# Kernel tuning notes

Measured on AMD Instinct MI355X. Metric: run time of the kernel, lower is better.

## Reference

```python
import jax, jax.numpy as jnp
import numpy as np

B, S, T = 4, 512, 512
V, D, F, H, DK, N = 32000, 512, 2048, 8, 64, 6
PAD = 0

# sinusoidal positional encoding table, matching the torch source exactly
_pos = np.arange(max(S, T))[:, None]
_i = np.arange(D // 2)[None, :]
_ang = _pos / (10000.0 ** (2 * _i / D))
_pe = np.empty((max(S, T), D), dtype=np.float32)
_pe[:, 0::2] = np.sin(_ang)
_pe[:, 1::2] = np.cos(_ang)
PE = jnp.asarray(_pe)


def setup_inputs() -> dict:
    key = jax.random.key(0)
    ks = iter(jax.random.split(key, 64))
    s = 0.02
    w = lambda shape: jax.random.normal(next(ks), shape, jnp.float32) * s
    inp = {
        'src': jax.random.randint(next(ks), (B, S), 0, V, jnp.int32),
        'trg': jax.random.randint(next(ks), (B, T), 0, V, jnp.int32),
        'emb_src': w((V, D)).at[PAD].set(0.0),
        'emb_trg': w((V, D)).at[PAD].set(0.0),
        # encoder stacks (leading axis = layer)
        'enc_wq': w((N, D, H * DK)), 'enc_wk': w((N, D, H * DK)),
        'enc_wv': w((N, D, H * DK)), 'enc_wo': w((N, H * DK, D)),
        'enc_ln1_g': jnp.ones((N, D)), 'enc_ln1_b': jnp.zeros((N, D)),
        'enc_w1': w((N, D, F)), 'enc_b1': jnp.zeros((N, F)),
        'enc_w2': w((N, F, D)), 'enc_b2': jnp.zeros((N, D)),
        'enc_ln2_g': jnp.ones((N, D)), 'enc_ln2_b': jnp.zeros((N, D)),
        # decoder stacks
        'dec_wq': w((N, D, H * DK)), 'dec_wk': w((N, D, H * DK)),
        'dec_wv': w((N, D, H * DK)), 'dec_wo': w((N, H * DK, D)),
        'dec_ln1_g': jnp.ones((N, D)), 'dec_ln1_b': jnp.zeros((N, D)),
        'dec_cq': w((N, D, H * DK)), 'dec_ck': w((N, D, H * DK)),
        'dec_cv': w((N, D, H * DK)), 'dec_co': w((N, H * DK, D)),
        'dec_ln2_g': jnp.ones((N, D)), 'dec_ln2_b': jnp.zeros((N, D)),
        'dec_w1': w((N, D, F)), 'dec_b1': jnp.zeros((N, F)),
        'dec_w2': w((N, F, D)), 'dec_b2': jnp.zeros((N, D)),
        'dec_ln3_g': jnp.ones((N, D)), 'dec_ln3_b': jnp.zeros((N, D)),
        'proj': w((D, V)),
    }
    return inp


def _ln(x, g, b, eps=1e-5):
    m = x.mean(-1, keepdims=True)
    v = ((x - m) ** 2).mean(-1, keepdims=True)
    return (x - m) * jax.lax.rsqrt(v + eps) * g + b


def _mha(xq, xkv, wq, wk, wv, wo, mask):
    b, lq, _ = xq.shape
    lk = xkv.shape[1]
    q = (xq @ wq).reshape(b, lq, H, DK).transpose(0, 2, 1, 3)   # bhqd
    k = (xkv @ wk).reshape(b, lk, H, DK).transpose(0, 2, 1, 3)  # bhkd
    v = (xkv @ wv).reshape(b, lk, H, DK).transpose(0, 2, 1, 3)  # bhkd
    scores = jnp.einsum('bhqd,bhkd->bhqk', q, k)
    scores = jnp.where(mask, -jnp.inf, scores)
    attn = jax.nn.softmax(scores * (DK ** -0.5), axis=-1)
    out = jnp.einsum('bhqk,bhkd->bhqd', attn, v)
    out = out.transpose(0, 2, 1, 3).reshape(b, lq, H * DK)
    return out @ wo


def _ffn(x, w1, b1, w2, b2):
    return jax.nn.relu(x @ w1 + b1) @ w2 + b2


def reference(src, trg, emb_src, emb_trg,
              enc_wq, enc_wk, enc_wv, enc_wo, enc_ln1_g, enc_ln1_b,
              enc_w1, enc_b1, enc_w2, enc_b2, enc_ln2_g, enc_ln2_b,
              dec_wq, dec_wk, dec_wv, dec_wo, dec_ln1_g, dec_ln1_b,
              dec_cq, dec_ck, dec_cv, dec_co, dec_ln2_g, dec_ln2_b,
              dec_w1, dec_b1, dec_w2, dec_b2, dec_ln3_g, dec_ln3_b,
              proj):
    scale = D ** 0.5
    src_pad = (src == PAD)[:, None, None, :]                 # [B,1,1,S]
    trg_pad = (trg == PAD)[:, None, None, :]                 # [B,1,1,T]
    causal = jnp.triu(jnp.ones((T, T), bool), 1)[None, None]  # [1,1,T,T]
    trg_mask = trg_pad | causal

    # encoder (dropout = identity in eval)
    x = emb_src[src] * scale + PE[None, :S]

    def enc_step(h, p):
        wq, wk, wv, wo, g1, b1, w1, bb1, w2, bb2, g2, b2 = p
        h = _ln(h + _mha(h, h, wq, wk, wv, wo, src_pad), g1, b1)
        h = _ln(h + _ffn(h, w1, bb1, w2, bb2), g2, b2)
        return h, None

    x_enc, _ = jax.lax.scan(enc_step, x,
        (enc_wq, enc_wk, enc_wv, enc_wo, enc_ln1_g, enc_ln1_b,
         enc_w1, enc_b1, enc_w2, enc_b2, enc_ln2_g, enc_ln2_b))

    # decoder
    y = emb_trg[trg] * scale + PE[None, :T]

    def dec_step(h, p):
        (wq, wk, wv, wo, g1, b1, cq, ck, cv, co, g2, b2,
         w1, bb1, w2, bb2, g3, b3) = p
        h = _ln(h + _mha(h, h, wq, wk, wv, wo, trg_mask), g1, b1)
        h = _ln(h + _mha(h, x_enc, cq, ck, cv, co, src_pad), g2, b2)
        h = _ln(h + _ffn(h, w1, bb1, w2, bb2), g3, b3)
        return h, None

    y, _ = jax.lax.scan(dec_step, y,
        (dec_wq, dec_wk, dec_wv, dec_wo, dec_ln1_g, dec_ln1_b,
         dec_cq, dec_ck, dec_cv, dec_co, dec_ln2_g, dec_ln2_b,
         dec_w1, dec_b1, dec_w2, dec_b2, dec_ln3_g, dec_ln3_b))

    return y @ proj  # [B, T, trg_vocab]
```

## Files before the change

### kernel.cpp

```cpp
#include <hip/hip_runtime.h>
#include <math.h>

#define BBATCH 4
#define SS 512
#define DDIM 512
#define FFN 2048
#define NHEAD 8
#define DHEAD 64
#define NL 6
#define NVOC 32000
#define MTOK (BBATCH*SS)
#define PAD_ID 0
#define MSZE ((size_t)MTOK * DDIM)

typedef unsigned short u16;
typedef __attribute__((ext_vector_type(8))) short short8;
typedef __attribute__((ext_vector_type(4))) float f32x4;

__device__ __forceinline__ u16 f2bf(float f) {
    union { float f; unsigned u; } v; v.f = f;
    unsigned r = ((v.u >> 16) & 1u) + 0x7fffu;
    return (u16)((v.u + r) >> 16);
}

__device__ __forceinline__ void gload16(const u16* g, u16* l) {
    __builtin_amdgcn_global_load_lds(
        (const __attribute__((address_space(1))) void*)g,
        (__attribute__((address_space(3))) void*)l, 16, 0, 0);
}

template<int N> __device__ __forceinline__ void waitv() {
    if constexpr (N == 0)      asm volatile("s_waitcnt vmcnt(0)" ::: "memory");
    else if constexpr (N == 2) asm volatile("s_waitcnt vmcnt(2)" ::: "memory");
    else if constexpr (N == 3) asm volatile("s_waitcnt vmcnt(3)" ::: "memory");
    else if constexpr (N == 4) asm volatile("s_waitcnt vmcnt(4)" ::: "memory");
    else if constexpr (N == 6) asm volatile("s_waitcnt vmcnt(6)" ::: "memory");
    else if constexpr (N == 8) asm volatile("s_waitcnt vmcnt(8)" ::: "memory");
    __builtin_amdgcn_sched_barrier(0);
}
__device__ __forceinline__ void rawbar() {
    __builtin_amdgcn_s_barrier();
    __builtin_amdgcn_sched_barrier(0);
}

template<int BM, int BN, int OUTBF, int RELU, int BIAS>
__device__ __forceinline__ void gemm_core(
    u16* __restrict__ AsB, u16* __restrict__ BsB,
    const u16* __restrict__ A, int lda,
    const u16* __restrict__ B, int ldb,
    void* __restrict__ Cv, int ldc,
    int row0, int col0, int K, const float* __restrict__ bias)
{
    const int tid  = threadIdx.x;
    const int lane = tid & 63;
    const int wid  = tid >> 6;
    const int wr   = wid >> 1, wc = wid & 1;
    constexpr int MF = BM / 32, NF = BN / 32, RA = BM / 64, RB = BN / 64;
// ... 102 lines not shown
        int nwg = gridDim.x * gridDim.y;
        int lin = by * gridDim.x + bx;
        int cpx = nwg >> 3;
        int s = (lin & 7) * cpx + (lin >> 3);
        bx = s % gridDim.x; by = s / gridDim.x;
    }
    const int zb = blockIdx.z >> 3, zh = blockIdx.z & 7;
    const u16* Ab = A + (size_t)zb * aSb + (size_t)zh * aSh;
    const u16* Bb = B + (size_t)zb * bSb + (size_t)zh * bSh;
    void* Cb = OUTBF ? (void*)((u16*)Cv + (size_t)zb * cSb + (size_t)zh * cSh)
                     : (void*)((float*)Cv + (size_t)zb * cSb + (size_t)zh * cSh);
    gemm_core<BM, BN, OUTBF, RELU, BIAS>(As, Bs, Ab, lda, Bb, ldb, Cb, ldc,
                                          by * BM, bx * BN, K, bias);
}

template<int BM, int BN>
__global__ __launch_bounds__(256) void mgemm_dual(
    const u16* __restrict__ A1, int lda1, const u16* __restrict__ B1, int ldb1,
    u16* __restrict__ C1, int ldc1, int nx1, int nblk1,
    const u16* __restrict__ A2, int lda2, const u16* __restrict__ B2, int ldb2,
    u16* __restrict__ C2, int ldc2, int nx2,
    int K)
{
    __shared__ __align__(16) u16 As[4 * BM * 32];
    __shared__ __align__(16) u16 Bs[4 * BN * 32];
    int id = blockIdx.x;
    if (id < nblk1) {
        gemm_core<BM, BN, 1, 0, 0>(As, Bs, A1, lda1, B1, ldb1, C1, ldc1,
                                    (id / nx1) * BM, (id % nx1) * BN, K, nullptr);
    } else {
        id -= nblk1;
        gemm_core<BM, BN, 1, 0, 0>(As, Bs, A2, lda2, B2, ldb2, C2, ldc2,
                                    (id / nx2) * BM, (id % nx2) * BN, K, nullptr);
    }
}

template<int CAUSAL>
__global__ __launch_bounds__(512) void flash_attn(
    const u16* __restrict__ Qp, int ldq,
    const u16* __restrict__ Kp, int ldk,
    const u16* __restrict__ Vtp,
    u16* __restrict__ O,
    const int* __restrict__ ids)
{
    __shared__ __align__(16) u16 Kl[3][64 * 64];
    __shared__ __align__(16) u16 Vl[3][64 * 64];
    __shared__ __align__(16) u16 Pl[8][16 * 64];
    __shared__ float msk[SS];

    const int tid = threadIdx.x, lane = tid & 63, wid = tid >> 6;
    const int bh = blockIdx.y, b = bh >> 3, h = bh & 7;
    const int q0 = blockIdx.x * 128;

    for (int i = tid; i < SS; i += 512)
        msk[i] = (ids[b * SS + i] == PAD_ID) ? -1e30f : 0.0f;

    const int qloc = wid * 16 + (lane & 15);
    const u16* Qb = Qp + (size_t)(b * SS + q0 + qloc) * ldq + h * 64 + ((lane >> 4) * 8);
    short8 qf[2];
    qf[0] = *(const short8*)(Qb);
    qf[1] = *(const short8*)(Qb + 32);

    const u16* Kb = Kp + (size_t)b * SS * ldk + h * 64;
    const u16* Vb = Vtp + (size_t)(h * 64) * MTOK + b * SS;

    auto stage = [&](int buf, int kt) {
        int row = tid >> 3;
        int sl  = tid & 7;
        int ls = sl ^ (row & 7);
        gload16(Kb + (size_t)(kt * 64 + row) * ldk + ls * 8, &Kl[buf][row * 64 + sl * 8]);
        gload16(Vb + (size_t)row * MTOK + kt * 64 + ls * 8, &Vl[buf][row * 64 + sl * 8]);
    };

    const int nt = CAUSAL ? (2 * blockIdx.x + 2) : (SS / 64);

    float m_i[4], l_i[4];
    f32x4 o_acc[4];
    const f32x4 zero = {0.f, 0.f, 0.f, 0.f};
    #pragma unroll
    for (int i = 0; i < 4; i++) { m_i[i] = -1e30f; l_i[i] = 0.0f; }
    #pragma unroll
    for (int n = 0; n < 4; n++) o_acc[n] = zero;

    auto comp = [&](int kt) {
        const int cur = kt % 3;
        f32x4 s_acc[4];
        #pragma unroll
        for (int n = 0; n < 4; n++) s_acc[n] = zero;
        __builtin_amdgcn_s_setprio(1);
        #pragma unroll
        for (int kk = 0; kk < 2; kk++) {
            #pragma unroll
            for (int n = 0; n < 4; n++) {
                int row = n * 16 + (lane & 15);
                int ls = (kk * 4 + (lane >> 4)) ^ (row & 7);
                short8 kf = *(const short8*)&Kl[cur][row * 64 + ls * 8];
                s_acc[n] = __builtin_amdgcn_mfma_f32_16x16x32_bf16(qf[kk], kf, s_acc[n], 0, 0, 0);
            }
        }
        __builtin_amdgcn_s_setprio(0);

        float sv[4][4];
        #pragma unroll
        for (int n = 0; n < 4; n++) {
            int kg = kt * 64 + n * 16 + (lane & 15);
            float mk = msk[kg];
            #pragma unroll
            for (int i = 0; i < 4; i++) {
                float s = s_acc[n][i] * 0.125f + mk;
                if (CAUSAL) {
                    int qg = q0 + wid * 16 + ((lane >> 4) << 2) + i;
// ... 29 lines not shown
                ps[i] += __shfl_xor(ps[i], msh);
            l_i[i] = l_i[i] * rs[i] + ps[i];
        }
        #pragma unroll
        for (int n = 0; n < 4; n++)
            #pragma unroll
            for (int i = 0; i < 4; i++)
                o_acc[n][i] *= rs[i];

        #pragma unroll
        for (int n = 0; n < 4; n++) {
            int k = n * 16 + (lane & 15);
            #pragma unroll
            for (int i = 0; i < 4; i++) {
                int q = ((lane >> 4) << 2) + i;
                Pl[wid][q * 64 + (((k >> 3) ^ (q & 7)) << 3) + (k & 7)] = f2bf(p[n][i]);
            }
        }
        asm volatile("s_waitcnt lgkmcnt(0)" ::: "memory");
        __builtin_amdgcn_sched_barrier(0);

        __builtin_amdgcn_s_setprio(1);
        #pragma unroll
        for (int kk = 0; kk < 2; kk++) {
            int qrow = lane & 15;
            int lsp = (kk * 4 + (lane >> 4)) ^ (qrow & 7);
            short8 pa = *(const short8*)&Pl[wid][qrow * 64 + lsp * 8];
            #pragma unroll
            for (int nf = 0; nf < 4; nf++) {
                int row = nf * 16 + (lane & 15);
                int vs = (kk * 4 + (lane >> 4)) ^ (row & 7);
                short8 vf = *(const short8*)&Vl[cur][row * 64 + vs * 8];
                o_acc[nf] = __builtin_amdgcn_mfma_f32_16x16x32_bf16(pa, vf, o_acc[nf], 0, 0, 0);
            }
        }
        __builtin_amdgcn_s_setprio(0);
    };

    stage(0, 0);
    stage(1, 1);
    int t = 0;
    for (; t < nt - 1; ++t) {
        waitv<2>();
        rawbar();
        if (t + 2 < nt) stage((t + 2) % 3, t + 2);
        comp(t);
    }
    waitv<0>(); rawbar(); comp(nt - 1);

    #pragma unroll
    for (int nf = 0; nf < 4; nf++) {
        int d = h * 64 + nf * 16 + (lane & 15);
        #pragma unroll
        for (int i = 0; i < 4; i++) {
            int qg = b * SS + q0 + wid * 16 + ((lane >> 4) << 2) + i;
            O[(size_t)qg * DDIM + d] = f2bf(o_acc[nf][i] / l_i[i]);
        }
    }
}

__device__ __forceinline__ void transp_core(const float* __restrict__ src, u16* __restrict__ dst,
                                            int N, int K, int n0, int k0)
{
    __shared__ u16 t[64][65];
    const int tid = threadIdx.x;
    #pragma unroll
    for (int i = 0; i < 16; i++) {
        int idx = tid + i * 256;
        int kr = idx >> 6, nc = idx & 63;
        t[kr][nc] = f2bf(src[(size_t)(k0 + kr) * N + n0 + nc]);
    }
    __syncthreads();
    #pragma unroll
    for (int i = 0; i < 16; i++) {
        int idx = tid + i * 256;
        int nr = idx >> 6, kc = idx & 63;
        dst[(size_t)(n0 + nr) * K + k0 + kc] = t[kc][nr];
    }
}

__global__ __launch_bounds__(256) void transp(const float* __restrict__ src, u16* __restrict__ dst,
                                              int N, int K, size_t sStride, size_t dStride)
{
    transp_core(src + (size_t)blockIdx.z * sStride, dst + (size_t)blockIdx.z * dStride,
                N, K, blockIdx.x * 64, blockIdx.y * 64);
}

#define OFF_QK 0u
#define OFF_WV 524288u
#define OFF_WO 786432u
#define OFF_CQ 1048576u
#define OFF_CK 1310720u
#define OFF_CV 1572864u
#define OFF_CO 1835008u
#define OFF_W1 2097152u
#define OFF_W2 3145728u
#define WBLK   4194304u
#define M2CNT  262144u
#define MF1CNT 1048576u

__global__ __launch_bounds__(256) void transpW(
    const float* p0, const float* p1, const float* p2, const float* p3,
    const float* p4, const float* p5, const float* p6, const float* p7,
    const float* p8, const float* p9, const float* p10, const float* p11,
    u16* __restrict__ wreg)
{
    int z = blockIdx.z;
    int w = z % 12, l = z / 12;
    const float* ptrs[12] = {p0,p1,p2,p3,p4,p5,p6,p7,p8,p9,p10,p11};
    const float* src = ptrs[w] + (size_t)l * M2CNT;
    u16* dst = wreg + (w < 4 ? (size_t)l * WBLK + (size_t)w * M2CNT
                             : (size_t)(NL + l) * WBLK + (size_t)(w - 4) * M2CNT);
    transp_core(src, dst, 512, 512, blockIdx.x * 64, blockIdx.y * 64);
}

// ... 3 lines not shown
    int z = blockIdx.z; int l = z % NL, w = z / NL;
    const float* src = (w ? d : e) + (size_t)l * MF1CNT;
    u16* dst = wreg + (size_t)(w * NL + l) * WBLK + OFF_W1;
    transp_core(src, dst, 2048, 512, blockIdx.x * 64, blockIdx.y * 64);
}

__global__ __launch_bounds__(256) void transpF2(const float* __restrict__ e,
                                                const float* __restrict__ d, u16* __restrict__ wreg)
{
    int z = blockIdx.z; int l = z % NL, w = z / NL;
    const float* src = (w ? d : e) + (size_t)l * MF1CNT;
    u16* dst = wreg + (size_t)(w * NL + l) * WBLK + OFF_W2;
    transp_core(src, dst, 512, 2048, blockIdx.x * 64, blockIdx.y * 64);
}

__global__ void pe_kernel(float* __restrict__ PEt)
{
    int pos = blockIdx.x, d = threadIdx.x;
    int i = d >> 1;
    double freq = exp(-(2.0 * (double)i / (double)DDIM) * log(10000.0));
    double ang = (double)pos * freq;
    PEt[pos * DDIM + d] = (float)((d & 1) ? cos(ang) : sin(ang));
}

__global__ void embed_kernel(const int* __restrict__ src, const int* __restrict__ trg,
                             const float* __restrict__ es, const float* __restrict__ et,
                             const float* __restrict__ PEt,
                             float* __restrict__ X, u16* __restrict__ Xb,
                             float* __restrict__ Y, u16* __restrict__ Ybf)
{
    int gtok = blockIdx.x;
    int d = threadIdx.x;
    bool dec = gtok >= MTOK;
    int tok = dec ? gtok - MTOK : gtok;
    int pos = tok & (SS - 1);
    int id = (dec ? trg : src)[tok];
    const float* emb = dec ? et : es;
    float val = emb[(size_t)id * DDIM + d] * 22.62741699796952f + PEt[pos * DDIM + d];
    (dec ? Y : X)[(size_t)tok * DDIM + d] = val;
    (dec ? Ybf : Xb)[(size_t)tok * DDIM + d] = f2bf(val);
}

__global__ __launch_bounds__(256) void add_ln_kernel(float* __restrict__ x,
    const float* __restrict__ addv, const float* __restrict__ g,
    const float* __restrict__ bta, u16* __restrict__ xb)
{
    int row = blockIdx.x;
    int tid = threadIdx.x;
    size_t base = (size_t)row * DDIM;
    __shared__ float sbuf[4];

    float v0 = x[base + tid]       + addv[base + tid];
    float v1 = x[base + tid + 256] + addv[base + tid + 256];

    float s = v0 + v1;
    #pragma unroll
    for (int o = 32; o > 0; o >>= 1) s += __shfl_down(s, o);
    if ((tid & 63) == 0) sbuf[tid >> 6] = s;
    __syncthreads();
    float mean = (sbuf[0] + sbuf[1] + sbuf[2] + sbuf[3]) * (1.0f / DDIM);
    __syncthreads();

    float d0 = v0 - mean, d1 = v1 - mean;
    float ss = d0 * d0 + d1 * d1;
    #pragma unroll
    for (int o = 32; o > 0; o >>= 1) ss += __shfl_down(ss, o);
    if ((tid & 63) == 0) sbuf[tid >> 6] = ss;
    __syncthreads();
    float var = (sbuf[0] + sbuf[1] + sbuf[2] + sbuf[3]) * (1.0f / DDIM);
    float inv = rsqrtf(var + 1e-5f);

    float o0 = d0 * inv * g[tid]       + bta[tid];
    float o1 = d1 * inv * g[tid + 256] + bta[tid + 256];
    x[base + tid] = o0;
    x[base + tid + 256] = o1;
    xb[base + tid] = f2bf(o0);
    xb[base + tid + 256] = f2bf(o1);
}

__global__ __launch_bounds__(256) void add_ln_red(float* __restrict__ x,
    const float* __restrict__ part, const float* __restrict__ bias,
    const float* __restrict__ g, const float* __restrict__ bta, u16* __restrict__ xb)
{
    int row = blockIdx.x;
    int tid = threadIdx.x;
    size_t base = (size_t)row * DDIM;
    __shared__ float sbuf[4];

    float v0 = x[base + tid]       + bias[tid];
    float v1 = x[base + tid + 256] + bias[tid + 256];
    #pragma unroll
    for (int s4 = 0; s4 < 4; s4++) {
        v0 += part[s4 * MSZE + base + tid];
        v1 += part[s4 * MSZE + base + tid + 256];
    }

    float s = v0 + v1;
    #pragma unroll
    for (int o = 32; o > 0; o >>= 1) s += __shfl_down(s, o);
    if ((tid & 63) == 0) sbuf[tid >> 6] = s;
    __syncthreads();
    float mean = (sbuf[0] + sbuf[1] + sbuf[2] + sbuf[3]) * (1.0f / DDIM);
    __syncthreads();

    float d0 = v0 - mean, d1 = v1 - mean;
    float ss = d0 * d0 + d1 * d1;
    #pragma unroll
    for (int o = 32; o > 0; o >>= 1) ss += __shfl_down(ss, o);
    if ((tid & 63) == 0) sbuf[tid >> 6] = ss;
    __syncthreads();
    float var = (sbuf[0] + sbuf[1] + sbuf[2] + sbuf[3]) * (1.0f / DDIM);
    float inv = rsqrtf(var + 1e-5f);

    float o0 = d0 * inv * g[tid]       + bta[tid];
    float o1 = d1 * inv * g[tid + 256] + bta[tid + 256];
    x[base + tid] = o0;
    x[base + tid + 256] = o1;
    xb[base + tid] = f2bf(o0);
    xb[base + tid + 256] = f2bf(o1);
}

extern "C" void kernel_launch(void* const* d_in, const int* in_sizes, int n_in,
                              void* d_out, int out_size, void* d_ws, size_t ws_size,
                              hipStream_t stream)
{
    (void)in_sizes; (void)n_in; (void)out_size;

    const int*   src      = (const int*)  d_in[0];
    const int*   trg      = (const int*)  d_in[1];
    const float* emb_src  = (const float*)d_in[2];
    const float* emb_trg  = (const float*)d_in[3];
    const float* enc_wq   = (const float*)d_in[4];
    const float* enc_wk   = (const float*)d_in[5];
    const float* enc_wv   = (const float*)d_in[6];
// ... 20 lines not shown
    const float* dec_ln2b = (const float*)d_in[27];
    const float* dec_w1   = (const float*)d_in[28];
    const float* dec_b1   = (const float*)d_in[29];
    const float* dec_w2   = (const float*)d_in[30];
    const float* dec_b2   = (const float*)d_in[31];
    const float* dec_ln3g = (const float*)d_in[32];
    const float* dec_ln3b = (const float*)d_in[33];
    const float* proj     = (const float*)d_in[34];

    float* OUT = (float*)d_out;
    char* base = (char*)d_ws;

    size_t off = 0;
    auto carve = [&](size_t bytes) { char* p = base + off; off += (bytes + 255) & ~(size_t)255; return p; };

    float* X      = (float*)carve(MSZE * 4);
    float* Yb     = (float*)carve(MSZE * 4);
    float* T1     = (float*)carve(MSZE * 4);
    u16*   Xb     = (u16*)  carve(MSZE * 2);
    u16*   Ybf    = (u16*)  carve(MSZE * 2);
    u16*   QKb    = (u16*)  carve((size_t)MTOK * 1024 * 2);
    u16*   Vt     = (u16*)  carve((size_t)512 * MTOK * 2);
    u16*   CTX    = (u16*)  carve(MSZE * 2);
    u16*   HFF    = (u16*)  carve((size_t)MTOK * FFN * 2);
    u16*   Kcr    = (u16*)  carve((size_t)NL * MTOK * 512 * 2);
    u16*   Vtc    = (u16*)  carve((size_t)NL * 512 * MTOK * 2);
    u16*   projT  = (u16*)  carve((size_t)NVOC * 512 * 2);
    float* PEt    = (float*)carve((size_t)SS * DDIM * 4);
    float* Tp4    = (float*)carve((size_t)4 * MSZE * 4);

    const size_t WFULL_B = (size_t)12 * WBLK * 2;
    bool full = (ws_size >= off + WFULL_B);
    u16* Wreg = (u16*)carve(full ? WFULL_B : (size_t)WBLK * 2);

    auto T = [&](const float* s, u16* d, int Kd, int Nd, size_t ss, size_t ds, int L) {
        transp<<<dim3(Nd / 64, Kd / 64, L), 256, 0, stream>>>(s, d, Nd, Kd, ss, ds);
    };

    pe_kernel<<<SS, DDIM, 0, stream>>>(PEt);
    T(proj, projT, 512, NVOC, 0, 0, 1);
    if (full) {
        transpW<<<dim3(8, 8, 12 * NL), 256, 0, stream>>>(
            enc_wq, enc_wk, enc_wv, enc_wo,
            dec_wq, dec_wk, dec_wv, dec_wo,
            dec_cq, dec_ck, dec_cv, dec_co, Wreg);
        transpF1<<<dim3(32, 8, 2 * NL), 256, 0, stream>>>(enc_w1, dec_w1, Wreg);
        transpF2<<<dim3(8, 32, 2 * NL), 256, 0, stream>>>(enc_w2, dec_w2, Wreg);
    }
    embed_kernel<<<2 * MTOK, DDIM, 0, stream>>>(src, trg, emb_src, emb_trg, PEt, X, Xb, Yb, Ybf);

    auto self_attn = [&](const u16* xsrc, const u16* wb, const int* mask_ids, int causal) {
        mgemm_dual<128, 128><<<dim3(192), 256, 0, stream>>>(
            xsrc, 512, wb + OFF_QK, 512, QKb, 1024, 8, 128,
            wb + OFF_WV, 512, xsrc, 512, Vt, MTOK, 16,
            512);
        if (causal)
            flash_attn<1><<<dim3(4, 32), 512, 0, stream>>>(QKb, 1024, QKb + 512, 1024, Vt, CTX, mask_ids);
        else
            flash_attn<0><<<dim3(4, 32), 512, 0, stream>>>(QKb, 1024, QKb + 512, 1024, Vt, CTX, mask_ids);
        mgemm<64, 64, 0, 0, 0><<<dim3(8, 32, 1), 256, 0, stream>>>(
            CTX, 512, 0, 0, wb + OFF_WO, 512, 0, 0, T1, 512, 0, 0, 512, nullptr);
    };

    auto ffn = [&](const u16* xsrc, const u16* wb, const float* b1) {
        mgemm<128, 128, 1, 1, 1><<<dim3(16, 16, 1), 256, 0, stream>>>(
            xsrc, 512, 0, 0, wb + OFF_W1, 512, 0, 0, HFF, FFN, 0, 0, 512, b1);
        mgemm<128, 128, 0, 0, 0><<<dim3(4, 16, 4), 256, 0, stream>>>(
            HFF, 2048, 0, 512, wb + OFF_W2, 2048, 0, 512,
            Tp4, 512, 0, MSZE, 512, nullptr);
    };

    const size_t M2 = M2CNT, MF1 = MF1CNT;

    for (int l = 0; l < NL; l++) {
        u16* wb;
        if (full) wb = Wreg + (size_t)l * WBLK;
        else {
            wb = Wreg;
            T(enc_wq + l * M2,  wb + OFF_QK,          512, 512,  0, 0, 1);
            T(enc_wk + l * M2,  wb + OFF_QK + M2,     512, 512,  0, 0, 1);
            T(enc_wv + l * M2,  wb + OFF_WV,          512, 512,  0, 0, 1);
            T(enc_wo + l * M2,  wb + OFF_WO,          512, 512,  0, 0, 1);
            T(enc_w1 + l * MF1, wb + OFF_W1,          512, 2048, 0, 0, 1);
            T(enc_w2 + l * MF1, wb + OFF_W2,          2048, 512, 0, 0, 1);
        }
        self_attn(Xb, wb, src, 0);
        add_ln_kernel<<<MTOK, 256, 0, stream>>>(X, T1, enc_ln1g + l * DDIM, enc_ln1b + l * DDIM, Xb);
        ffn(Xb, wb, enc_b1 + l * FFN);
        add_ln_red<<<MTOK, 256, 0, stream>>>(X, Tp4, enc_b2 + l * DDIM,
                                             enc_ln2g + l * DDIM, enc_ln2b + l * DDIM, Xb);
    }

    if (full) {
        u16* Wd = Wreg + (size_t)NL * WBLK;
        mgemm<128, 128, 1, 0, 0><<<dim3(4, 16, NL), 256, 0, stream>>>(
            Xb, 512, 0, 0, Wd + OFF_CK, 512, 0, WBLK, Kcr, 512, 0, (size_t)MTOK * 512, 512, nullptr);
        mgemm<128, 128, 1, 0, 0><<<dim3(16, 4, NL), 256, 0, stream>>>(
            Wd + OFF_CV, 512, 0, WBLK, Xb, 512, 0, 0, Vtc, MTOK, 0, (size_t)512 * MTOK, 512, nullptr);
    }

    for (int l = 0; l < NL; l++) {
        u16* wb;
        if (full) wb = Wreg + (size_t)(NL + l) * WBLK;
        else {
            wb = Wreg;
            T(dec_wq + l * M2,  wb + OFF_QK,          512, 512,  0, 0, 1);
            T(dec_wk + l * M2,  wb + OFF_QK + M2,     512, 512,  0, 0, 1);
            T(dec_wv + l * M2,  wb + OFF_WV,          512, 512,  0, 0, 1);
            T(dec_wo + l * M2,  wb + OFF_WO,          512, 512,  0, 0, 1);
            T(dec_cq + l * M2,  wb + OFF_CQ,          512, 512,  0, 0, 1);
            T(dec_ck + l * M2,  wb + OFF_CK,          512, 512,  0, 0, 1);
            T(dec_cv + l * M2,  wb + OFF_CV,          512, 512,  0, 0, 1);
            T(dec_co + l * M2,  wb + OFF_CO,          512, 512,  0, 0, 1);
            T(dec_w1 + l * MF1, wb + OFF_W1,          512, 2048, 0, 0, 1);
            T(dec_w2 + l * MF1, wb + OFF_W2,          2048, 512, 0, 0, 1);
            mgemm<128, 128, 1, 0, 0><<<dim3(4, 16, 1), 256, 0, stream>>>(
                Xb, 512, 0, 0, wb + OFF_CK, 512, 0, 0, Kcr + (size_t)l * MTOK * 512, 512, 0, 0, 512, nullptr);
            mgemm<128, 128, 1, 0, 0><<<dim3(16, 4, 1), 256, 0, stream>>>(
                wb + OFF_CV, 512, 0, 0, Xb, 512, 0, 0, Vtc + (size_t)l * 512 * MTOK, MTOK, 0, 0, 512, nullptr);
        }
        self_attn(Ybf, wb, trg, 1);
        add_ln_kernel<<<MTOK, 256, 0, stream>>>(Yb, T1, dec_ln1g + l * DDIM, dec_ln1b + l * DDIM, Ybf);
        mgemm<64, 64, 1, 0, 0><<<dim3(8, 32, 1), 256, 0, stream>>>(
            Ybf, 512, 0, 0, wb + OFF_CQ, 512, 0, 0, QKb, 1024, 0, 0, 512, nullptr);
        flash_attn<0><<<dim3(4, 32), 512, 0, stream>>>(
            QKb, 1024, Kcr + (size_t)l * MTOK * 512, 512, Vtc + (size_t)l * 512 * MTOK, CTX, src);
        mgemm<64, 64, 0, 0, 0><<<dim3(8, 32, 1), 256, 0, stream>>>(
            CTX, 512, 0, 0, wb + OFF_CO, 512, 0, 0, T1, 512, 0, 0, 512, nullptr);
        add_ln_kernel<<<MTOK, 256, 0, stream>>>(Yb, T1, dec_ln2g + l * DDIM, dec_ln2b + l * DDIM, Ybf);
        ffn(Ybf, wb, dec_b1 + l * FFN);
        add_ln_red<<<MTOK, 256, 0, stream>>>(Yb, Tp4, dec_b2 + l * DDIM,
                                             dec_ln3g + l * DDIM, dec_ln3b + l * DDIM, Ybf);
    }

    mgemm<128, 128, 0, 0, 0, 1><<<dim3(NVOC / 128, 16, 1), 256, 0, stream>>>(
        Ybf, 512, 0, 0, projT, 512, 0, 0, OUT, NVOC, 0, 0, 512, nullptr);
}
```

Before: 1.547 ms.

## Fuse each encoder/decoder layer into one persistent kernel with grid barriers

Replaces the per-layer chain of separate GEMM, flash-attention and layernorm launches with a single 256-block persistent kernel per layer. Phases are separated by atomic-counter grid barriers in global memory. Flash attention is reworked to 256 threads and 64-row query tiles so it fits the same block shape, and the positional-encoding kernel is removed from the launch sequence. This is meant to cut launch overhead and inter-kernel gaps, at the cost of spin-wait barriers that need all 256 blocks co-resident and of less flexible per-phase tiling.

```diff
diff --git a/kernel.cpp b/kernel.cpp
--- a/kernel.cpp
+++ b/kernel.cpp
@@ -32,15 +32,25 @@
 template<int N> __device__ __forceinline__ void waitv() {
     if constexpr (N == 0)      asm volatile("s_waitcnt vmcnt(0)" ::: "memory");
     else if constexpr (N == 2) asm volatile("s_waitcnt vmcnt(2)" ::: "memory");
-    else if constexpr (N == 3) asm volatile("s_waitcnt vmcnt(3)" ::: "memory");
     else if constexpr (N == 4) asm volatile("s_waitcnt vmcnt(4)" ::: "memory");
-    else if constexpr (N == 6) asm volatile("s_waitcnt vmcnt(6)" ::: "memory");
     else if constexpr (N == 8) asm volatile("s_waitcnt vmcnt(8)" ::: "memory");
     __builtin_amdgcn_sched_barrier(0);
 }
 __device__ __forceinline__ void rawbar() {
     __builtin_amdgcn_s_barrier();
     __builtin_amdgcn_sched_barrier(0);
+}
+
+__device__ __forceinline__ void gbar(unsigned* c) {
+    __threadfence();
+    __syncthreads();
+    if (threadIdx.x == 0) {
+        __hip_atomic_fetch_add(c, 1u, __ATOMIC_ACQ_REL, __HIP_MEMORY_SCOPE_AGENT);
+        while (__hip_atomic_load(c, __ATOMIC_ACQUIRE, __HIP_MEMORY_SCOPE_AGENT) < 256u)
+            __builtin_amdgcn_s_sleep(2);
+        __threadfence();
+    }
+    __syncthreads();
 }
 
 template<int BM, int BN, int OUTBF, int RELU, int BIAS>
@@ -173,45 +183,23 @@
                                           by * BM, bx * BN, K, bias);
 }
 
-template<int BM, int BN>
-__global__ __launch_bounds__(256) void mgemm_dual(
-    const u16* __restrict__ A1, int lda1, const u16* __restrict__ B1, int ldb1,
-    u16* __restrict__ C1, int ldc1, int nx1, int nblk1,
-    const u16* __restrict__ A2, int lda2, const u16* __restrict__ B2, int ldb2,
-    u16* __restrict__ C2, int ldc2, int nx2,
-    int K)
-{
-    __shared__ __align__(16) u16 As[4 * BM * 32];
-    __shared__ __align__(16) u16 Bs[4 * BN * 32];
-    int id = blockIdx.x;
-    if (id < nblk1) {
-        gemm_core<BM, BN, 1, 0, 0>(As, Bs, A1, lda1, B1, ldb1, C1, ldc1,
-                                    (id / nx1) * BM, (id % nx1) * BN, K, nullptr);
-    } else {
-        id -= nblk1;
-        gemm_core<BM, BN, 1, 0, 0>(As, Bs, A2, lda2, B2, ldb2, C2, ldc2,
-                                    (id / nx2) * BM, (id % nx2) * BN, K, nullptr);
-    }
-}
-
 template<int CAUSAL>
-__global__ __launch_bounds__(512) void flash_attn(
+__device__ void flash_phase(char* smem, int qt, int bh,
     const u16* __restrict__ Qp, int ldq,
     const u16* __restrict__ Kp, int ldk,
     const u16* __restrict__ Vtp,
-    u16* __restrict__ O,
-    const int* __restrict__ ids)
-{
-    __shared__ __align__(16) u16 Kl[3][64 * 64];
-    __shared__ __align__(16) u16 Vl[3][64 * 64];
-    __shared__ __align__(16) u16 Pl[8][16 * 64];
-    __shared__ float msk[SS];
+    u16* __restrict__ O, const int* __restrict__ ids)
+{
+    u16* Kl = (u16*)smem;
+    u16* Vl = Kl + 12288;
+    u16* Pl = Vl + 12288;
+    float* msk = (float*)(Pl + 4096);
 
     const int tid = threadIdx.x, lane = tid & 63, wid = tid >> 6;
-    const int bh = blockIdx.y, b = bh >> 3, h = bh & 7;
-    const int q0 = blockIdx.x * 128;
-
-    for (int i = tid; i < SS; i += 512)
+    const int b = bh >> 3, h = bh & 7;
+    const int q0 = qt * 64;
+
+    for (int i = tid; i < SS; i += 256)
         msk[i] = (ids[b * SS + i] == PAD_ID) ? -1e30f : 0.0f;
 
     const int qloc = wid * 16 + (lane & 15);
@@ -220,18 +208,22 @@
     qf[0] = *(const short8*)(Qb);
     qf[1] = *(const short8*)(Qb + 32);
 
-    const u16* Kb = Kp + (size_t)b * SS * ldk + h * 64;
+    const u16* Kb = Qp == Kp ? Kp : Kp;
+    Kb = Kp + (size_t)b * SS * ldk + h * 64;
     const u16* Vb = Vtp + (size_t)(h * 64) * MTOK + b * SS;
 
     auto stage = [&](int buf, int kt) {
-        int row = tid >> 3;
-        int sl  = tid & 7;
-        int ls = sl ^ (row & 7);
-        gload16(Kb + (size_t)(kt * 64 + row) * ldk + ls * 8, &Kl[buf][row * 64 + sl * 8]);
-        gload16(Vb + (size_t)row * MTOK + kt * 64 + ls * 8, &Vl[buf][row * 64 + sl * 8]);
+        int row = tid >> 3, sl = tid & 7;
+        #pragma unroll
+        for (int r = 0; r < 2; r++) {
+            int rr = row + r * 32;
+            int ls = sl ^ (rr & 7);
+            gload16(Kb + (size_t)(kt * 64 + rr) * ldk + ls * 8, &Kl[buf * 4096 + rr * 64 + sl * 8]);
+            gload16(Vb + (size_t)rr * MTOK + kt * 64 + ls * 8, &Vl[buf * 4096 + rr * 64 + sl * 8]);
+        }
     };
 
-    const int nt = CAUSAL ? (2 * blockIdx.x + 2) : (SS / 64);
+    const int nt = CAUSAL ? (qt + 1) : (SS / 64);
 
     float m_i[4], l_i[4];
     f32x4 o_acc[4];
@@ -253,7 +245,7 @@
             for (int n = 0; n < 4; n++) {
                 int row = n * 16 + (lane & 15);
                 int ls = (kk * 4 + (lane >> 4)) ^ (row & 7);
-                short8 kf = *(const short8*)&Kl[cur][row * 64 + ls * 8];
+                short8 kf = *(const short8*)&Kl[cur * 4096 + row * 64 + ls * 8];
                 s_acc[n] = __builtin_amdgcn_mfma_f32_16x16x32_bf16(qf[kk], kf, s_acc[n], 0, 0, 0);
             }
         }
@@ -313,7 +305,7 @@
             #pragma unroll
             for (int i = 0; i < 4; i++) {
                 int q = ((lane >> 4) << 2) + i;
-                Pl[wid][q * 64 + (((k >> 3) ^ (q & 7)) << 3) + (k & 7)] = f2bf(p[n][i]);
+                Pl[wid * 1024 + q * 64 + (((k >> 3) ^ (q & 7)) << 3) + (k & 7)] = f2bf(p[n][i]);
             }
         }
         asm volatile("s_waitcnt lgkmcnt(0)" ::: "memory");
@@ -324,12 +316,12 @@
         for (int kk = 0; kk < 2; kk++) {
             int qrow = lane & 15;
             int lsp = (kk * 4 + (lane >> 4)) ^ (qrow & 7);
-            short8 pa = *(const short8*)&Pl[wid][qrow * 64 + lsp * 8];
+            short8 pa = *(const short8*)&Pl[wid * 1024 + qrow * 64 + lsp * 8];
             #pragma unroll
             for (int nf = 0; nf < 4; nf++) {
                 int row = nf * 16 + (lane & 15);
                 int vs = (kk * 4 + (lane >> 4)) ^ (row & 7);
-                short8 vf = *(const short8*)&Vl[cur][row * 64 + vs * 8];
+                short8 vf = *(const short8*)&Vl[cur * 4096 + row * 64 + vs * 8];
                 o_acc[nf] = __builtin_amdgcn_mfma_f32_16x16x32_bf16(pa, vf, o_acc[nf], 0, 0, 0);
             }
         }
@@ -340,7 +332,7 @@
     stage(1, 1);
     int t = 0;
     for (; t < nt - 1; ++t) {
-        waitv<2>();
+        waitv<4>();
         rawbar();
         if (t + 2 < nt) stage((t + 2) % 3, t + 2);
         comp(t);
@@ -358,31 +350,77 @@
     }
 }
 
-__device__ __forceinline__ void transp_core(const float* __restrict__ src, u16* __restrict__ dst,
-                                            int N, int K, int n0, int k0)
-{
-    __shared__ u16 t[64][65];
+__device__ void ln8(float* __restrict__ x, const float* __restrict__ addv,
+    const float* __restrict__ g, const float* __restrict__ bta,
+    u16* __restrict__ xb, int jid, float* sbuf)
+{
     const int tid = threadIdx.x;
-    #pragma unroll
-    for (int i = 0; i < 16; i++) {
-        int idx = tid + i * 256;
-        int kr = idx >> 6, nc = idx & 63;
-        t[kr][nc] = f2bf(src[(size_t)(k0 + kr) * N + n0 + nc]);
-    }
-    __syncthreads();
-    #pragma unroll
-    for (int i = 0; i < 16; i++) {
-        int idx = tid + i * 256;
-        int nr = idx >> 6, kc = idx & 63;
-        dst[(size_t)(n0 + nr) * K + k0 + kc] = t[kc][nr];
-    }
-}
-
-__global__ __launch_bounds__(256) void transp(const float* __restrict__ src, u16* __restrict__ dst,
-                                              int N, int K, size_t sStride, size_t dStride)
-{
-    transp_core(src + (size_t)blockIdx.z * sStride, dst + (size_t)blockIdx.z * dStride,
-                N, K, blockIdx.x * 64, blockIdx.y * 64);
+    for (int r = 0; r < 8; r++) {
+        size_t base = (size_t)(jid * 8 + r) * DDIM;
+        float v0 = x[base + tid]       + addv[base + tid];
+        float v1 = x[base + tid + 256] + addv[base + tid + 256];
+        float s = v0 + v1;
+        #pragma unroll
+        for (int o = 32; o > 0; o >>= 1) s += __shfl_down(s, o);
+        if ((tid & 63) == 0) sbuf[tid >> 6] = s;
+        __syncthreads();
+        float mean = (sbuf[0] + sbuf[1] + sbuf[2] + sbuf[3]) * (1.0f / DDIM);
+        __syncthreads();
+        float d0 = v0 - mean, d1 = v1 - mean;
+        float ss = d0 * d0 + d1 * d1;
+        #pragma unroll
+        for (int o = 32; o > 0; o >>= 1) ss += __shfl_down(ss, o);
+        if ((tid & 63) == 0) sbuf[tid >> 6] = ss;
+        __syncthreads();
+        float var = (sbuf[0] + sbuf[1] + sbuf[2] + sbuf[3]) * (1.0f / DDIM);
+        float inv = rsqrtf(var + 1e-5f);
+        float o0 = d0 * inv * g[tid]       + bta[tid];
+        float o1 = d1 * inv * g[tid + 256] + bta[tid + 256];
+        x[base + tid] = o0;
+        x[base + tid + 256] = o1;
+        xb[base + tid] = f2bf(o0);
+        xb[base + tid + 256] = f2bf(o1);
+        __syncthreads();
+    }
+}
+
+__device__ void ln_red8(float* __restrict__ x, const float* __restrict__ part,
+    const float* __restrict__ bias, const float* __restrict__ g,
+    const float* __restrict__ bta, u16* __restrict__ xb, int jid, float* sbuf)
+{
+    const int tid = threadIdx.x;
+    for (int r = 0; r < 8; r++) {
+        size_t base = (size_t)(jid * 8 + r) * DDIM;
+        float v0 = x[base + tid]       + bias[tid];
+        float v1 = x[base + tid + 256] + bias[tid + 256];
+        #pragma unroll
+        for (int s4 = 0; s4 < 4; s4++) {
+            v0 += part[s4 * MSZE + base + tid];
+            v1 += part[s4 * MSZE + base + tid + 256];
+        }
+        float s = v0 + v1;
+        #pragma unroll
+        for (int o = 32; o > 0; o >>= 1) s += __shfl_down(s, o);
+        if ((tid & 63) == 0) sbuf[tid >> 6] = s;
+        __syncthreads();
+        float mean = (sbuf[0] + sbuf[1] + sbuf[2] + sbuf[3]) * (1.0f / DDIM);
+        __syncthreads();
+        float d0 = v0 - mean, d1 = v1 - mean;
+        float ss = d0 * d0 + d1 * d1;
+        #pragma unroll
+        for (int o = 32; o > 0; o >>= 1) ss += __shfl_down(ss, o);
+        if ((tid & 63) == 0) sbuf[tid >> 6] = ss;
+        __syncthreads();
+        float var = (sbuf[0] + sbuf[1] + sbuf[2] + sbuf[3]) * (1.0f / DDIM);
+        float inv = rsqrtf(var + 1e-5f);
+        float o0 = d0 * inv * g[tid]       + bta[tid];
+        float o1 = d1 * inv * g[tid + 256] + bta[tid + 256];
+        x[base + tid] = o0;
+        x[base + tid + 256] = o1;
+        xb[base + tid] = f2bf(o0);
+        xb[base + tid + 256] = f2bf(o1);
+        __syncthreads();
+    }
 }
 
 #define OFF_QK 0u
@@ -398,6 +436,125 @@
 #define M2CNT  262144u
 #define MF1CNT 1048576u
 
+__global__ __launch_bounds__(256) void enc_layer(
+    u16* __restrict__ Xb_, float* __restrict__ X_,
+    const u16* __restrict__ wb,
+    const float* __restrict__ b1, const float* __restrict__ b2,
+    const float* __restrict__ ln1g, const float* __restrict__ ln1b,
+    const float* __restrict__ ln2g, const float* __restrict__ ln2b,
+    u16* __restrict__ QKb, u16* __restrict__ Vt, u16* __restrict__ CTX,
+    float* __restrict__ T1, u16* __restrict__ HFF, float* __restrict__ Tp4,
+    const int* __restrict__ ids, unsigned* __restrict__ bar)
+{
+    __shared__ __align__(16) char smem[65536];
+    __shared__ float sbuf[4];
+    u16* A_ = (u16*)smem;  u16* B_ = A_ + 16384;
+    u16* A64 = (u16*)smem; u16* B64 = A64 + 8192;
+    const int jid = blockIdx.x;
+
+    if (jid < 128)
+        gemm_core<128,128,1,0,0>(A_, B_, Xb_, 512, wb + OFF_QK, 512, QKb, 1024,
+                                 (jid >> 3) * 128, (jid & 7) * 128, 512, nullptr);
+    else if (jid < 192)
+        gemm_core<128,128,1,0,0>(A_, B_, wb + OFF_WV, 512, Xb_, 512, Vt, MTOK,
+                                 ((jid - 128) >> 4) * 128, ((jid - 128) & 15) * 128, 512, nullptr);
+    gbar(bar + 0);
+    flash_phase<0>(smem, jid & 7, jid >> 3, QKb, 1024, QKb + 512, 1024, Vt, CTX, ids);
+    gbar(bar + 1);
+    gemm_core<64,64,0,0,0>(A64, B64, CTX, 512, wb + OFF_WO, 512, T1, 512,
+                           (jid >> 3) * 64, (jid & 7) * 64, 512, nullptr);
+    gbar(bar + 2);
+    ln8(X_, T1, ln1g, ln1b, Xb_, jid, sbuf);
+    gbar(bar + 3);
+    gemm_core<128,128,1,1,1>(A_, B_, Xb_, 512, wb + OFF_W1, 512, HFF, FFN,
+                             (jid >> 4) * 128, (jid & 15) * 128, 512, b1);
+    gbar(bar + 4);
+    { int s = jid >> 6, rem = jid & 63;
+      gemm_core<128,128,0,0,0>(A_, B_, HFF + s * 512, 2048, wb + OFF_W2 + s * 512, 2048,
+                               Tp4 + (size_t)s * MSZE, 512, (rem >> 2) * 128, (rem & 3) * 128, 512, nullptr); }
+    gbar(bar + 5);
+    ln_red8(X_, Tp4, b2, ln2g, ln2b, Xb_, jid, sbuf);
+}
+
+__global__ __launch_bounds__(256) void dec_layer(
+    u16* __restrict__ Ybf_, float* __restrict__ Y_,
+    const u16* __restrict__ wb,
+    const float* __restrict__ b1, const float* __restrict__ b2,
+    const float* __restrict__ ln1g, const float* __restrict__ ln1b,
+    const float* __restrict__ ln2g, const float* __restrict__ ln2b,
+    const float* __restrict__ ln3g, const float* __restrict__ ln3b,
+    const u16* __restrict__ Kcr_l, const u16* __restrict__ Vtc_l,
+    u16* __restrict__ QKb, u16* __restrict__ Vt, u16* __restrict__ CTX,
+    float* __restrict__ T1, u16* __restrict__ HFF, float* __restrict__ Tp4,
+    const int* __restrict__ trg, const int* __restrict__ srcids, unsigned* __restrict__ bar)
+{
+    __shared__ __align__(16) char smem[65536];
+    __shared__ float sbuf[4];
+    u16* A_ = (u16*)smem;  u16* B_ = A_ + 16384;
+    u16* A64 = (u16*)smem; u16* B64 = A64 + 8192;
+    const int jid = blockIdx.x;
+
+    if (jid < 128)
+        gemm_core<128,128,1,0,0>(A_, B_, Ybf_, 512, wb + OFF_QK, 512, QKb, 1024,
+                                 (jid >> 3) * 128, (jid & 7) * 128, 512, nullptr);
+    else if (jid < 192)
+        gemm_core<128,128,1,0,0>(A_, B_, wb + OFF_WV, 512, Ybf_, 512, Vt, MTOK,
+                                 ((jid - 128) >> 4) * 128, ((jid - 128) & 15) * 128, 512, nullptr);
+    gbar(bar + 0);
+    flash_phase<1>(smem, jid & 7, jid >> 3, QKb, 1024, QKb + 512, 1024, Vt, CTX, trg);
+    gbar(bar + 1);
+    gemm_core<64,64,0,0,0>(A64, B64, CTX, 512, wb + OFF_WO, 512, T1, 512,
+                           (jid >> 3) * 64, (jid & 7) * 64, 512, nullptr);
+    gbar(bar + 2);
+    ln8(Y_, T1, ln1g, ln1b, Ybf_, jid, sbuf);
+    gbar(bar + 3);
+    gemm_core<64,64,1,0,0>(A64, B64, Ybf_, 512, wb + OFF_CQ, 512, QKb, 1024,
+                           (jid >> 3) * 64, (jid & 7) * 64, 512, nullptr);
+    gbar(bar + 4);
+    flash_phase<0>(smem, jid & 7, jid >> 3, QKb, 1024, Kcr_l, 512, Vtc_l, CTX, srcids);
+    gbar(bar + 5);
+    gemm_core<64,64,0,0,0>(A64, B64, CTX, 512, wb + OFF_CO, 512, T1, 512,
+                           (jid >> 3) * 64, (jid & 7) * 64, 512, nullptr);
+    gbar(bar + 6);
+    ln8(Y_, T1, ln2g, ln2b, Ybf_, jid, sbuf);
+    gbar(bar + 7);
+    gemm_core<128,128,1,1,1>(A_, B_, Ybf_, 512, wb + OFF_W1, 512, HFF, FFN,
+                             (jid >> 4) * 128, (jid & 15) * 128, 512, b1);
+    gbar(bar + 8);
+    { int s = jid >> 6, rem = jid & 63;
+      gemm_core<128,128,0,0,0>(A_, B_, HFF + s * 512, 2048, wb + OFF_W2 + s * 512, 2048,
+                               Tp4 + (size_t)s * MSZE, 512, (rem >> 2) * 128, (rem & 3) * 128, 512, nullptr); }
+    gbar(bar + 9);
+    ln_red8(Y_, Tp4, b2, ln3g, ln3b, Ybf_, jid, sbuf);
+}
+
+__device__ __forceinline__ void transp_core(const float* __restrict__ src, u16* __restrict__ dst,
+                                            int N, int K, int n0, int k0)
+{
+    __shared__ u16 t[64][65];
+    const int tid = threadIdx.x;
+    #pragma unroll
+    for (int i = 0; i < 16; i++) {
+        int idx = tid + i * 256;
+        int kr = idx >> 6, nc = idx & 63;
+        t[kr][nc] = f2bf(src[(size_t)(k0 + kr) * N + n0 + nc]);
+    }
+    __syncthreads();
+    #pragma unroll
+    for (int i = 0; i < 16; i++) {
+        int idx = tid + i * 256;
+        int nr = idx >> 6, kc = idx & 63;
+        dst[(size_t)(n0 + nr) * K + k0 + kc] = t[kc][nr];
+    }
+}
+
+__global__ __launch_bounds__(256) void transp(const float* __restrict__ src, u16* __restrict__ dst,
+                                              int N, int K, size_t sStride, size_t dStride)
+{
+    transp_core(src + (size_t)blockIdx.z * sStride, dst + (size_t)blockIdx.z * dStride,
+                N, K, blockIdx.x * 64, blockIdx.y * 64);
+}
+
 __global__ __launch_bounds__(256) void transpW(
     const float* p0, const float* p1, const float* p2, const float* p3,
     const float* p4, const float* p5, const float* p6, const float* p7,
@@ -431,18 +588,8 @@
     transp_core(src, dst, 512, 2048, blockIdx.x * 64, blockIdx.y * 64);
 }
 
-__global__ void pe_kernel(float* __restrict__ PEt)
-{
-    int pos = blockIdx.x, d = threadIdx.x;
-    int i = d >> 1;
-    double freq = exp(-(2.0 * (double)i / (double)DDIM) * log(10000.0));
-    double ang = (double)pos * freq;
-    PEt[pos * DDIM + d] = (float)((d & 1) ? cos(ang) : sin(ang));
-}
-
 __global__ void embed_kernel(const int* __restrict__ src, const int* __restrict__ trg,
                              const float* __restrict__ es, const float* __restrict__ et,
-                             const float* __restrict__ PEt,
                              float* __restrict__ X, u16* __restrict__ Xb,
                              float* __restrict__ Y, u16* __restrict__ Ybf)
 {
@@ -453,88 +600,13 @@
     int pos = tok & (SS - 1);
     int id = (dec ? trg : src)[tok];
     const float* emb = dec ? et : es;
-    float val = emb[(size_t)id * DDIM + d] * 22.62741699796952f + PEt[pos * DDIM + d];
+    int i = d >> 1;
+    double freq = exp(-(2.0 * (double)i / (double)DDIM) * log(10000.0));
+    double ang = (double)pos * freq;
+    float pe = (float)((d & 1) ? cos(ang) : sin(ang));
+    float val = emb[(size_t)id * DDIM + d] * 22.62741699796952f + pe;
     (dec ? Y : X)[(size_t)tok * DDIM + d] = val;
     (dec ? Ybf : Xb)[(size_t)tok * DDIM + d] = f2bf(val);
-}
-
-__global__ __launch_bounds__(256) void add_ln_kernel(float* __restrict__ x,
-    const float* __restrict__ addv, const float* __restrict__ g,
-    const float* __restrict__ bta, u16* __restrict__ xb)
-{
-    int row = blockIdx.x;
-    int tid = threadIdx.x;
-    size_t base = (size_t)row * DDIM;
-    __shared__ float sbuf[4];
-
-    float v0 = x[base + tid]       + addv[base + tid];
-    float v1 = x[base + tid + 256] + addv[base + tid + 256];
-
-    float s = v0 + v1;
-    #pragma unroll
-    for (int o = 32; o > 0; o >>= 1) s += __shfl_down(s, o);
-    if ((tid & 63) == 0) sbuf[tid >> 6] = s;
-    __syncthreads();
-    float mean = (sbuf[0] + sbuf[1] + sbuf[2] + sbuf[3]) * (1.0f / DDIM);
-    __syncthreads();
-
-    float d0 = v0 - mean, d1 = v1 - mean;
-    float ss = d0 * d0 + d1 * d1;
-    #pragma unroll
-    for (int o = 32; o > 0; o >>= 1) ss += __shfl_down(ss, o);
-    if ((tid & 63) == 0) sbuf[tid >> 6] = ss;
-    __syncthreads();
-    float var = (sbuf[0] + sbuf[1] + sbuf[2] + sbuf[3]) * (1.0f / DDIM);
-    float inv = rsqrtf(var + 1e-5f);
-
-    float o0 = d0 * inv * g[tid]       + bta[tid];
-    float o1 = d1 * inv * g[tid + 256] + bta[tid + 256];
-    x[base + tid] = o0;
-    x[base + tid + 256] = o1;
-    xb[base + tid] = f2bf(o0);
-    xb[base + tid + 256] = f2bf(o1);
-}
-
-__global__ __launch_bounds__(256) void add_ln_red(float* __restrict__ x,
-    const float* __restrict__ part, const float* __restrict__ bias,
-    const float* __restrict__ g, const float* __restrict__ bta, u16* __restrict__ xb)
-{
-    int row = blockIdx.x;
-    int tid = threadIdx.x;
-    size_t base = (size_t)row * DDIM;
-    __shared__ float sbuf[4];
-
-    float v0 = x[base + tid]       + bias[tid];
-    float v1 = x[base + tid + 256] + bias[tid + 256];
-    #pragma unroll
-    for (int s4 = 0; s4 < 4; s4++) {
-        v0 += part[s4 * MSZE + base + tid];
-        v1 += part[s4 * MSZE + base + tid + 256];
-    }
-
-    float s = v0 + v1;
-    #pragma unroll
-    for (int o = 32; o > 0; o >>= 1) s += __shfl_down(s, o);
-    if ((tid & 63) == 0) sbuf[tid >> 6] = s;
-    __syncthreads();
-    float mean = (sbuf[0] + sbuf[1] + sbuf[2] + sbuf[3]) * (1.0f / DDIM);
-    __syncthreads();
-
-    float d0 = v0 - mean, d1 = v1 - mean;
-    float ss = d0 * d0 + d1 * d1;
-    #pragma unroll
-    for (int o = 32; o > 0; o >>= 1) ss += __shfl_down(ss, o);
-    if ((tid & 63) == 0) sbuf[tid >> 6] = ss;
-    __syncthreads();
-    float var = (sbuf[0] + sbuf[1] + sbuf[2] + sbuf[3]) * (1.0f / DDIM);
-    float inv = rsqrtf(var + 1e-5f);
-
-    float o0 = d0 * inv * g[tid]       + bta[tid];
-    float o1 = d1 * inv * g[tid + 256] + bta[tid + 256];
-    x[base + tid] = o0;
-    x[base + tid + 256] = o1;
-    xb[base + tid] = f2bf(o0);
-    xb[base + tid + 256] = f2bf(o1);
 }
 
 extern "C" void kernel_launch(void* const* d_in, const int* in_sizes, int n_in,
@@ -585,20 +657,20 @@
     size_t off = 0;
     auto carve = [&](size_t bytes) { char* p = base + off; off += (bytes + 255) & ~(size_t)255; return p; };
 
-    float* X      = (float*)carve(MSZE * 4);
-    float* Yb     = (float*)carve(MSZE * 4);
-    float* T1     = (float*)carve(MSZE * 4);
-    u16*   Xb     = (u16*)  carve(MSZE * 2);
-    u16*   Ybf    = (u16*)  carve(MSZE * 2);
-    u16*   QKb    = (u16*)  carve((size_t)MTOK * 1024 * 2);
-    u16*   Vt     = (u16*)  carve((size_t)512 * MTOK * 2);
-    u16*   CTX    = (u16*)  carve(MSZE * 2);
-    u16*   HFF    = (u16*)  carve((size_t)MTOK * FFN * 2);
-    u16*   Kcr    = (u16*)  carve((size_t)NL * MTOK * 512 * 2);
-    u16*   Vtc    = (u16*)  carve((size_t)NL * 512 * MTOK * 2);
-    u16*   projT  = (u16*)  carve((size_t)NVOC * 512 * 2);
-    float* PEt    = (float*)carve((size_t)SS * DDIM * 4);
-    float* Tp4    = (float*)carve((size_t)4 * MSZE * 4);
+    float*    X      = (float*)   carve(MSZE * 4);
+    float*    Yb     = (float*)   carve(MSZE * 4);
+    float*    T1     = (float*)   carve(MSZE * 4);
+    u16*      Xb     = (u16*)     carve(MSZE * 2);
+    u16*      Ybf    = (u16*)     carve(MSZE * 2);
+    u16*      QKb    = (u16*)     carve((size_t)MTOK * 1024 * 2);
+    u16*      Vt     = (u16*)     carve((size_t)512 * MTOK * 2);
+    u16*      CTX    = (u16*)     carve(MSZE * 2);
+    u16*      HFF    = (u16*)     carve((size_t)MTOK * FFN * 2);
+    u16*      Kcr    = (u16*)     carve((size_t)NL * MTOK * 512 * 2);
+    u16*      Vtc    = (u16*)     carve((size_t)NL * 512 * MTOK * 2);
+    u16*      projT  = (u16*)     carve((size_t)NVOC * 512 * 2);
+    float*    Tp4    = (float*)   carve((size_t)4 * MSZE * 4);
+    unsigned* Bar    = (unsigned*)carve(12 * 16 * sizeof(unsigned));
 
     const size_t WFULL_B = (size_t)12 * WBLK * 2;
     bool full = (ws_size >= off + WFULL_B);
@@ -608,7 +680,7 @@
         transp<<<dim3(Nd / 64, Kd / 64, L), 256, 0, stream>>>(s, d, Nd, Kd, ss, ds);
     };
 
-    pe_kernel<<<SS, DDIM, 0, stream>>>(PEt);
+    hipMemsetAsync(Bar, 0, 12 * 16 * sizeof(unsigned), stream);
     T(proj, projT, 512, NVOC, 0, 0, 1);
     if (full) {
         transpW<<<dim3(8, 8, 12 * NL), 256, 0, stream>>>(
@@ -618,28 +690,7 @@
         transpF1<<<dim3(32, 8, 2 * NL), 256, 0, stream>>>(enc_w1, dec_w1, Wreg);
         transpF2<<<dim3(8, 32, 2 * NL), 256, 0, stream>>>(enc_w2, dec_w2, Wreg);
     }
-    embed_kernel<<<2 * MTOK, DDIM, 0, stream>>>(src, trg, emb_src, emb_trg, PEt, X, Xb, Yb, Ybf);
-
-    auto self_attn = [&](const u16* xsrc, const u16* wb, const int* mask_ids, int causal) {
-        mgemm_dual<128, 128><<<dim3(192), 256, 0, stream>>>(
-            xsrc, 512, wb + OFF_QK, 512, QKb, 1024, 8, 128,
-            wb + OFF_WV, 512, xsrc, 512, Vt, MTOK, 16,
-            512);
-        if (causal)
-            flash_attn<1><<<dim3(4, 32), 512, 0, stream>>>(QKb, 1024, QKb + 512, 1024, Vt, CTX, mask_ids);
-        else
-            flash_attn<0><<<dim3(4, 32), 512, 0, stream>>>(QKb, 1024, QKb + 512, 1024, Vt, CTX, mask_ids);
-        mgemm<64, 64, 0, 0, 0><<<dim3(8, 32, 1), 256, 0, stream>>>(
-            CTX, 512, 0, 0, wb + OFF_WO, 512, 0, 0, T1, 512, 0, 0, 512, nullptr);
-    };
-
-    auto ffn = [&](const u16* xsrc, const u16* wb, const float* b1) {
-        mgemm<128, 128, 1, 1, 1><<<dim3(16, 16, 1), 256, 0, stream>>>(
-            xsrc, 512, 0, 0, wb + OFF_W1, 512, 0, 0, HFF, FFN, 0, 0, 512, b1);
-        mgemm<128, 128, 0, 0, 0><<<dim3(4, 16, 4), 256, 0, stream>>>(
-            HFF, 2048, 0, 512, wb + OFF_W2, 2048, 0, 512,
-            Tp4, 512, 0, MSZE, 512, nullptr);
-    };
+    embed_kernel<<<2 * MTOK, DDIM, 0, stream>>>(src, trg, emb_src, emb_trg, X, Xb, Yb, Ybf);
 
     const size_t M2 = M2CNT, MF1 = MF1CNT;
 
@@ -648,18 +699,16 @@
         if (full) wb = Wreg + (size_t)l * WBLK;
         else {
             wb = Wreg;
-            T(enc_wq + l * M2,  wb + OFF_QK,          512, 512,  0, 0, 1);
-            T(enc_wk + l * M2,  wb + OFF_QK + M2,     512, 512,  0, 0, 1);
-            T(enc_wv + l * M2,  wb + OFF_WV,          512, 512,  0, 0, 1);
-            T(enc_wo + l * M2,  wb + OFF_WO,          512, 512,  0, 0, 1);
-            T(enc_w1 + l * MF1, wb + OFF_W1,          512, 2048, 0, 0, 1);
-            T(enc_w2 + l * MF1, wb + OFF_W2,          2048, 512, 0, 0, 1);
-        }
-        self_attn(Xb, wb, src, 0);
-        add_ln_kernel<<<MTOK, 256, 0, stream>>>(X, T1, enc_ln1g + l * DDIM, enc_ln1b + l * DDIM, Xb);
-        ffn(Xb, wb, enc_b1 + l * FFN);
-        add_ln_red<<<MTOK, 256, 0, stream>>>(X, Tp4, enc_b2 + l * DDIM,
-                                             enc_ln2g + l * DDIM, enc_ln2b + l * DDIM, Xb);
+            T(enc_wq + l * M2,  wb + OFF_QK,      512, 512,  0, 0, 1);
+            T(enc_wk + l * M2,  wb + OFF_QK + M2, 512, 512,  0, 0, 1);
+            T(enc_wv + l * M2,  wb + OFF_WV,      512, 512,  0, 0, 1);
+            T(enc_wo + l * M2,  wb + OFF_WO,      512, 512,  0, 0, 1);
+            T(enc_w1 + l * MF1, wb + OFF_W1,      512, 2048, 0, 0, 1);
+            T(enc_w2 + l * MF1, wb + OFF_W2,      2048, 512, 0, 0, 1);
+        }
+        enc_layer<<<256, 256, 0, stream>>>(Xb, X, wb, enc_b1 + l * FFN, enc_b2 + l * DDIM,
+            enc_ln1g + l * DDIM, enc_ln1b + l * DDIM, enc_ln2g + l * DDIM, enc_ln2b + l * DDIM,
+            QKb, Vt, CTX, T1, HFF, Tp4, src, Bar + l * 16);
     }
 
     if (full) {
@@ -675,33 +724,26 @@
         if (full) wb = Wreg + (size_t)(NL + l) * WBLK;
         else {
             wb = Wreg;
-            T(dec_wq + l * M2,  wb + OFF_QK,          512, 512,  0, 0, 1);
-            T(dec_wk + l * M2,  wb + OFF_QK + M2,     512, 512,  0, 0, 1);
-            T(dec_wv + l * M2,  wb + OFF_WV,          512, 512,  0, 0, 1);
-            T(dec_wo + l * M2,  wb + OFF_WO,          512, 512,  0, 0, 1);
-            T(dec_cq + l * M2,  wb + OFF_CQ,          512, 512,  0, 0, 1);
-            T(dec_ck + l * M2,  wb + OFF_CK,          512, 512,  0, 0, 1);
-            T(dec_cv + l * M2,  wb + OFF_CV,          512, 512,  0, 0, 1);
-            T(dec_co + l * M2,  wb + OFF_CO,          512, 512,  0, 0, 1);
-            T(dec_w1 + l * MF1, wb + OFF_W1,          512, 2048, 0, 0, 1);
-            T(dec_w2 + l * MF1, wb + OFF_W2,          2048, 512, 0, 0, 1);
+            T(dec_wq + l * M2,  wb + OFF_QK,      512, 512,  0, 0, 1);
+            T(dec_wk + l * M2,  wb + OFF_QK + M2, 512, 512,  0, 0, 1);
+            T(dec_wv + l * M2,  wb + OFF_WV,      512, 512,  0, 0, 1);
+            T(dec_wo + l * M2,  wb + OFF_WO,      512, 512,  0, 0, 1);
+            T(dec_cq + l * M2,  wb + OFF_CQ,      512, 512,  0, 0, 1);
+            T(dec_ck + l * M2,  wb + OFF_CK,      512, 512,  0, 0, 1);
+            T(dec_cv + l * M2,  wb + OFF_CV,      512, 512,  0, 0, 1);
+            T(dec_co + l * M2,  wb + OFF_CO,      512, 512,  0, 0, 1);
+            T(dec_w1 + l * MF1, wb + OFF_W1,      512, 2048, 0, 0, 1);
+            T(dec_w2 + l * MF1, wb + OFF_W2,      2048, 512, 0, 0, 1);
             mgemm<128, 128, 1, 0, 0><<<dim3(4, 16, 1), 256, 0, stream>>>(
                 Xb, 512, 0, 0, wb + OFF_CK, 512, 0, 0, Kcr + (size_t)l * MTOK * 512, 512, 0, 0, 512, nullptr);
             mgemm<128, 128, 1, 0, 0><<<dim3(16, 4, 1), 256, 0, stream>>>(
                 wb + OFF_CV, 512, 0, 0, Xb, 512, 0, 0, Vtc + (size_t)l * 512 * MTOK, MTOK, 0, 0, 512, nullptr);
         }
-        self_attn(Ybf, wb, trg, 1);
-        add_ln_kernel<<<MTOK, 256, 0, stream>>>(Yb, T1, dec_ln1g + l * DDIM, dec_ln1b + l * DDIM, Ybf);
-        mgemm<64, 64, 1, 0, 0><<<dim3(8, 32, 1), 256, 0, stream>>>(
-            Ybf, 512, 0, 0, wb + OFF_CQ, 512, 0, 0, QKb, 1024, 0, 0, 512, nullptr);
-        flash_attn<0><<<dim3(4, 32), 512, 0, stream>>>(
-            QKb, 1024, Kcr + (size_t)l * MTOK * 512, 512, Vtc + (size_t)l * 512 * MTOK, CTX, src);
-        mgemm<64, 64, 0, 0, 0><<<dim3(8, 32, 1), 256, 0, stream>>>(
-            CTX, 512, 0, 0, wb + OFF_CO, 512, 0, 0, T1, 512, 0, 0, 512, nullptr);
-        add_ln_kernel<<<MTOK, 256, 0, stream>>>(Yb, T1, dec_ln2g + l * DDIM, dec_ln2b + l * DDIM, Ybf);
-        ffn(Ybf, wb, dec_b1 + l * FFN);
-        add_ln_red<<<MTOK, 256, 0, stream>>>(Yb, Tp4, dec_b2 + l * DDIM,
-                                             dec_ln3g + l * DDIM, dec_ln3b + l * DDIM, Ybf);
+        dec_layer<<<256, 256, 0, stream>>>(Ybf, Yb, wb, dec_b1 + l * FFN, dec_b2 + l * DDIM,
+            dec_ln1g + l * DDIM, dec_ln1b + l * DDIM, dec_ln2g + l * DDIM, dec_ln2b + l * DDIM,
+            dec_ln3g + l * DDIM, dec_ln3b + l * DDIM,
+            Kcr + (size_t)l * MTOK * 512, Vtc + (size_t)l * 512 * MTOK,
+            QKb, Vt, CTX, T1, HFF, Tp4, trg, src, Bar + (size_t)(6 + l) * 16);
     }
 
     mgemm<128, 128, 0, 0, 0, 1><<<dim3(NVOC / 128, 16, 1), 256, 0, stream>>>(
```

Measured after the change: 6.062 ms. +291.8%, slower.
